# Kernel optimization log

Measured on AMD Instinct MI355X. Metric: run time of the kernel, lower is better.

Reference implementation:

```python
import jax, jax.numpy as jnp
import numpy as np

B, N, DIM, IN_DIM, H = 8, 3136, 147, 64, 1
HD = IN_DIM // H          # per-head value/key dim = 64
MLP_HID = int(IN_DIM * 1.0)
EPS = 1e-5


def _ln(x, w, b):
    m = jnp.mean(x, axis=-1, keepdims=True)
    v = jnp.mean((x - m) ** 2, axis=-1, keepdims=True)
    return (x - m) / jnp.sqrt(v + EPS) * w + b


def setup_inputs() -> dict:
    key = jax.random.key(0)
    ks = jax.random.split(key, 12)
    r = lambda k, shp, s=0.02: (jax.random.normal(k, shp, dtype=jnp.float32) * s)
    return {
        "x": jax.random.normal(ks[0], (B, N, DIM), dtype=jnp.float32),
        "norm1_w": jnp.ones((DIM,), jnp.float32),
        "norm1_b": jnp.zeros((DIM,), jnp.float32),
        "qkv_w": r(ks[1], (3 * IN_DIM, DIM)),
        "scale": jnp.full((H,), (DIM // H) ** -0.5, dtype=jnp.float32),
        "proj_w": r(ks[2], (IN_DIM, IN_DIM)),
        "proj_b": jnp.zeros((IN_DIM,), jnp.float32),
        "norm2_w": jnp.ones((IN_DIM,), jnp.float32),
        "norm2_b": jnp.zeros((IN_DIM,), jnp.float32),
        "fc1_w": r(ks[3], (MLP_HID, IN_DIM)),
        "fc1_b": jnp.zeros((MLP_HID,), jnp.float32),
        "fc2_w": r(ks[4], (IN_DIM, MLP_HID)),
        "fc2_b": jnp.zeros((IN_DIM,), jnp.float32),
    }


def reference(x, norm1_w, norm1_b, qkv_w, scale, proj_w, proj_b,
              norm2_w, norm2_b, fc1_w, fc1_b, fc2_w, fc2_b):
    h = _ln(x, norm1_w, norm1_b)                               # [B,N,DIM]
    qkv = jnp.einsum('bnc,oc->bno', h, qkv_w)                  # [B,N,3*IN_DIM]
    qkv = qkv.reshape(B, N, 3, H, HD).transpose(2, 0, 3, 1, 4)  # [3,B,H,N,HD]
    q, k, v = qkv[0], qkv[1], qkv[2]
    # LMSA: learnable per-head scale + diagonal (self) exclusion mask
    attn = jnp.einsum('bhid,bhjd->bhij', q, k) * scale[None, :, None, None]
    eye = jnp.eye(N, dtype=bool)
    attn = jnp.where(eye[None, None], -jnp.inf, attn)
    attn = jax.nn.softmax(attn, axis=-1)
    o = jnp.einsum('bhij,bhjd->bhid', attn, v)                 # [B,H,N,HD]
    o = o.transpose(0, 2, 1, 3).reshape(B, N, IN_DIM)
    o = jnp.einsum('bnd,od->bno', o, proj_w) + proj_b
    # num_heads == 1 -> residual is v itself
    x_attn = v[:, 0] + o                                       # [B,N,IN_DIM]
    h2 = _ln(x_attn, norm2_w, norm2_b)
    h2 = jax.nn.gelu(jnp.einsum('bnd,hd->bnh', h2, fc1_w) + fc1_b,
                     approximate=False)
    h2 = jnp.einsum('bnh,oh->bno', h2, fc2_w) + fc2_b
    return x_attn + h2
```

## Files before the change

### kernel.cpp

```cpp
#include <hip/hip_runtime.h>
#include <math.h>

#define B_    8
#define N_    3136
#define DIM_  147
#define KP_   160
#define TOK_  (B_*N_)
#define QKV3_ 192

typedef __attribute__((ext_vector_type(4))) float f32x4;
typedef __attribute__((ext_vector_type(4))) unsigned int u32x4;
typedef __attribute__((ext_vector_type(8))) short short8;

static __device__ __forceinline__ unsigned short f2b(float f){
  unsigned int u = __float_as_uint(f);
  u += 0x7fffu + ((u >> 16) & 1u);
  return (unsigned short)(u >> 16);
}
static __device__ __forceinline__ unsigned short f2b_t(float f){
  return (unsigned short)(__float_as_uint(f) >> 16);
}

__global__ __launch_bounds__(256) void k_prep(const float* __restrict__ qkvw,
                                              const float* __restrict__ projw,
                                              const float* __restrict__ fc1w,
                                              const float* __restrict__ fc2w,
                                              unsigned short* __restrict__ wp,
                                              unsigned short* __restrict__ wpj,
                                              unsigned short* __restrict__ w1b,
                                              unsigned short* __restrict__ w2b){
  int idx = blockIdx.x*256 + threadIdx.x;
  if(idx < QKV3_*KP_){
    int n = idx / KP_, k = idx - n*KP_;
    wp[idx] = f2b((k < DIM_) ? qkvw[n*DIM_ + k] : 0.f);
  }
  if(idx < 4096){
    wpj[idx] = f2b(projw[idx]);
    w1b[idx] = f2b(fc1w[idx]);
    w2b[idx] = f2b(fc2w[idx]);
  }
}

__global__ __launch_bounds__(256) void k_ln1(const float* __restrict__ x,
                                             const float* __restrict__ w1,
                                             const float* __restrict__ b1,
                                             unsigned short* __restrict__ hn){
  int t    = blockIdx.x*4 + (threadIdx.x >> 6);
  int lane = threadIdx.x & 63;
  const float* xr = x + (size_t)t*DIM_;
  float x0 = xr[lane];
  float x1 = xr[lane+64];
  float x2 = (lane < 19) ? xr[lane+128] : 0.f;
  float s  = x0+x1+x2;
  float sq = x0*x0 + x1*x1 + x2*x2;
  for(int d=1; d<64; d<<=1){ s += __shfl_xor(s,d,64); sq += __shfl_xor(sq,d,64); }
  float mean = s * (1.f/DIM_);
  float var  = sq * (1.f/DIM_) - mean*mean;
  float rstd = rsqrtf(var + 1e-5f);
  unsigned short* hr = hn + (size_t)t*KP_;
  hr[lane]    = f2b((x0-mean)*rstd*w1[lane]    + b1[lane]);
  hr[lane+64] = f2b((x1-mean)*rstd*w1[lane+64] + b1[lane+64]);
  if(lane < 19)       hr[lane+128] = f2b((x2-mean)*rstd*w1[lane+128] + b1[lane+128]);
  else if(lane < 32)  hr[lane+128] = 0;
}

__global__ __launch_bounds__(256) void k_qkv(const unsigned short* __restrict__ hn,
                                             const unsigned short* __restrict__ wp,
                                             const float* __restrict__ scale,
                                             unsigned short* __restrict__ qb,
                                             unsigned short* __restrict__ kb,
                                             unsigned short* __restrict__ vtb,
                                             float* __restrict__ vf){
  __shared__ alignas(16) unsigned int Asm[64*20];
  __shared__ alignas(16) unsigned int Bsm[192*20];
  __shared__ alignas(16) unsigned short VT[64*72];
  int tid = threadIdx.x;
  int w = tid>>6, lane = tid&63, quad = lane>>4, l16 = lane&15;
  int m0 = blockIdx.x*64;
  const unsigned int* hn32 = (const unsigned int*)hn;
  const unsigned int* wp32 = (const unsigned int*)wp;
  float sc2 = scale[0] * 1.44269504089f;
  f32x4 acc[12];
  for(int i=0;i<12;i++) acc[i] = (f32x4){0.f,0.f,0.f,0.f};

  for(int kk=0; kk<5; kk++){
    __syncthreads();
    for(int rep=0; rep<4; rep++){
      int idx = rep*256 + tid;
      int row = idx>>4, col = idx&15;
      Asm[row*20+col] = hn32[(m0+row)*80 + kk*16 + col];
    }
    for(int rep=0; rep<12; rep++){
      int idx = rep*256 + tid;
      int row = idx>>4, col = idx&15;
      Bsm[row*20+col] = wp32[row*80 + kk*16 + col];
    }
    __syncthreads();
    short8 Af = *(const short8*)((const unsigned short*)Asm + (w*16+l16)*40 + quad*8);
    for(int nt=0; nt<12; nt++){
      short8 Bf = *(const short8*)((const unsigned short*)Bsm + (nt*16+l16)*40 + quad*8);
      acc[nt] = __builtin_amdgcn_mfma_f32_16x16x32_bf16(Af, Bf, acc[nt], 0,0,0);
    }
  }
  for(int nt=0; nt<12; nt++){
    int o = nt*16 + l16;
    for(int r=0; r<4; r++){
      int tl = w*16 + quad*4 + r;
      int mg = m0 + tl;
      float val = acc[nt][r];
      if(o < 64){
        qb[mg*64 + o] = f2b(val*sc2);
      } else if(o < 128){
        kb[mg*64 + (o-64)] = f2b(val);
      } else {
        int hd = o - 128;
        vf[mg*64 + hd] = val;
        VT[hd*72 + tl] = f2b(val);
      }
    }
  }
  __syncthreads();
  {
    int b = m0 / N_, n0 = m0 - b*N_;
    const unsigned int* VT32 = (const unsigned int*)VT;
    unsigned int* vg = (unsigned int*)vtb + (size_t)b*64*(N_/2) + n0/2;
    for(int rep=0; rep<8; rep++){
      int idx = rep*256 + tid; int row = idx>>5, col = idx&31;
      vg[row*(N_/2) + col] = VT32[row*36 + col];
    }
  }
}

__global__ __launch_bounds__(256) void k_attn(const unsigned short* __restrict__ qb,
                                              const unsigned short* __restrict__ kb,
                                              const unsigned short* __restrict__ vtb,
                                              float* __restrict__ Opart,
                                              float* __restrict__ lpart){
  __shared__ alignas(16) unsigned int Qs[64*36];
  __shared__ alignas(16) unsigned int Ks[64*36];
  __shared__ alignas(16) unsigned int Vs[64*36];
  __shared__ alignas(16) unsigned int Ps[64*36];
  int tid = threadIdx.x;
  int w = tid>>6, lane = tid&63, quad = lane>>4, l16 = lane&15;
  int qt = blockIdx.x, sp = blockIdx.y, b = blockIdx.z;
  int kv0 = sp*25, ntile = sp ? 24 : 25;

  {
    const u32x4* qg = (const u32x4*)(qb + ((size_t)b*N_ + qt*64)*64);
    for(int rep=0; rep<2; rep++){
      int idx = rep*256 + tid; int row = idx>>3, c4 = idx&7;
      *(u32x4*)&Qs[row*36 + c4*4] = qg[row*8 + c4];
    }
  }
  __syncthreads();
  short8 Qf[2];
  for(int kk=0; kk<2; kk++)
    Qf[kk] = *(const short8*)((const unsigned short*)Qs + (w*16+l16)*72 + kk*32 + quad*8);

  f32x4 O[4];
  for(int i=0;i<4;i++) O[i] = (f32x4){0.f,0.f,0.f,0.f};
  float lrow[4] = {0.f,0.f,0.f,0.f};
  unsigned short* Ph = (unsigned short*)Ps;

  for(int t=0; t<ntile; t++){
    int kvt = kv0 + t;
    __syncthreads();
    {
      const u32x4* kg = (const u32x4*)(kb + ((size_t)b*N_ + (size_t)kvt*64)*64);
      const u32x4* vg = (const u32x4*)vtb + (size_t)b*64*392 + (size_t)kvt*8;
      for(int rep=0; rep<2; rep++){
        int idx = rep*256 + tid; int row = idx>>3, c4 = idx&7;
        *(u32x4*)&Ks[row*36 + c4*4] = kg[row*8 + c4];
        *(u32x4*)&Vs[row*36 + c4*4] = vg[(size_t)row*392 + c4];
      }
    }
    __syncthreads();

    f32x4 S[4];
    for(int jt=0; jt<4; jt++){
      short8 Kf0 = *(const short8*)((const unsigned short*)Ks + (jt*16+l16)*72 + quad*8);
      short8 Kf1 = *(const short8*)((const unsigned short*)Ks + (jt*16+l16)*72 + 32 + quad*8);
      f32x4 z = (f32x4){0.f,0.f,0.f,0.f};
      z = __builtin_amdgcn_mfma_f32_16x16x32_bf16(Qf[0], Kf0, z, 0,0,0);
      S[jt] = __builtin_amdgcn_mfma_f32_16x16x32_bf16(Qf[1], Kf1, z, 0,0,0);
    }
    if(kvt == qt){
      for(int jt=0; jt<4; jt++){
        int c = jt*16 + l16;
        for(int r=0; r<4; r++){
          float p = (c == w*16+quad*4+r) ? 0.f : __builtin_amdgcn_exp2f(S[jt][r]);
          lrow[r] += p;
          Ph[(w*16+quad*4+r)*72 + c] = f2b_t(p);
        }
      }
    } else {
      for(int jt=0; jt<4; jt++){
        int c = jt*16 + l16;
        for(int r=0; r<4; r++){
          float p = __builtin_amdgcn_exp2f(S[jt][r]);
          lrow[r] += p;
          Ph[(w*16+quad*4+r)*72 + c] = f2b_t(p);
        }
      }
    }
    __asm__ volatile("" ::: "memory");
    short8 Pf0 = *(const short8*)(Ph + (w*16+l16)*72 + quad*8);
    short8 Pf1 = *(const short8*)(Ph + (w*16+l16)*72 + 32 + quad*8);
    for(int jt=0; jt<4; jt++){
      short8 Vf0 = *(const short8*)((const unsigned short*)Vs + (jt*16+l16)*72 + quad*8);
      short8 Vf1 = *(const short8*)((const unsigned short*)Vs + (jt*16+l16)*72 + 32 + quad*8);
      O[jt] = __builtin_amdgcn_mfma_f32_16x16x32_bf16(Pf0, Vf0, O[jt], 0,0,0);
      O[jt] = __builtin_amdgcn_mfma_f32_16x16x32_bf16(Pf1, Vf1, O[jt], 0,0,0);
    }
  }
  for(int r=0; r<4; r++){
    float lr = lrow[r];
    lr += __shfl_xor(lr,1,64); lr += __shfl_xor(lr,2,64);
    lr += __shfl_xor(lr,4,64); lr += __shfl_xor(lr,8,64);
    size_t tok = (size_t)b*N_ + qt*64 + w*16 + quad*4 + r;
    if(l16 == 0) lpart[(size_t)sp*TOK_ + tok] = lr;
    float* og = Opart + ((size_t)sp*TOK_ + tok)*64;
    for(int jt=0; jt<4; jt++) og[jt*16 + l16] = O[jt][r];
  }
}

__global__ __launch_bounds__(256) void k_mlp(const float* __restrict__ O0,
                                             const float* __restrict__ O1,
                                             const float* __restrict__ l0,
                                             const float* __restrict__ l1,
                                             const float* __restrict__ vf,
                                             const unsigned short* __restrict__ wpj,
                                             const unsigned short* __restrict__ w1b,
                                             const unsigned short* __restrict__ w2b,
                                             const float* __restrict__ projb,
                                             const float* __restrict__ n2w,
                                             const float* __restrict__ n2b,
                                             const float* __restrict__ fc1b,
                                             const float* __restrict__ fc2b,
                                             float* __restrict__ out){
  __shared__ alignas(16) unsigned int Wp32[64*36];
  __shared__ alignas(16) unsigned int W132[64*36];
  __shared__ alignas(16) unsigned int W232[64*36];
  __shared__ alignas(16) unsigned int Xs32[64*36];
  unsigned short* Wp = (unsigned short*)Wp32;
  unsigned short* W1 = (unsigned short*)W132;
  unsigned short* W2 = (unsigned short*)W232;
  unsigned short* Xs = (unsigned short*)Xs32;
  int tid = threadIdx.x;
  int w = tid>>6, lane = tid&63, quad = lane>>4, l16 = lane&15;
  int t0 = blockIdx.x*64;

  for(int rep=0; rep<2; rep++){
    int idx = rep*256 + tid; int row = idx>>3, c4 = idx&7;
    *(u32x4*)&Wp32[row*36+c4*4]  = ((const u32x4*)wpj)[row*8+c4];
    *(u32x4*)&W132[row*36+c4*4] = ((const u32x4*)w1b)[row*8+c4];
    *(u32x4*)&W232[row*36+c4*4] = ((const u32x4*)w2b)[row*8+c4];
  }
  {
    const f32x4* A0 = (const f32x4*)(O0 + (size_t)t0*64);
    const f32x4* A1 = (const f32x4*)(O1 + (size_t)t0*64);
    for(int rep=0; rep<4; rep++){
      int idx = rep*256 + tid; int row = idx>>4, c4 = idx&15;
      f32x4 a = A0[row*16+c4] + A1[row*16+c4];
      float linv = 1.f/(l0[t0+row] + l1[t0+row]);
      unsigned int p0 = ((unsigned int)f2b(a[1]*linv)<<16) | f2b(a[0]*linv);
      unsigned int p1 = ((unsigned int)f2b(a[3]*linv)<<16) | f2b(a[2]*linv);
      Xs32[row*36 + c4*2]     = p0;
      Xs32[row*36 + c4*2 + 1] = p1;
    }
  }
  __syncthreads();

  f32x4 acc[4];
  for(int i=0;i<4;i++) acc[i] = (f32x4){0.f,0.f,0.f,0.f};
  short8 Af[2];
  for(int kk=0; kk<2; kk++)
    Af[kk] = *(const short8*)(Xs + (w*16+l16)*72 + kk*32 + quad*8);
  for(int jt=0; jt<4; jt++)
    for(int kk=0; kk<2; kk++){
      short8 Bf = *(const short8*)(Wp + (jt*16+l16)*72 + kk*32 + quad*8);
      acc[jt] = __builtin_amdgcn_mfma_f32_16x16x32_bf16(Af[kk], Bf, acc[jt], 0,0,0);
    }
  float xa[4][4];
  for(int jt=0; jt<4; jt++){
    int col = jt*16 + l16;
    float pb = projb[col];
    for(int r=0; r<4; r++){
      int tg = t0 + w*16 + quad*4 + r;
      xa[jt][r] = acc[jt][r] + pb + vf[tg*64 + col];
    }
  }
  for(int r=0; r<4; r++){
    float s=0.f, sq=0.f;
    for(int jt=0; jt<4; jt++){ s += xa[jt][r]; sq += xa[jt][r]*xa[jt][r]; }
    s  += __shfl_xor(s,1,64);  s  += __shfl_xor(s,2,64);
    s  += __shfl_xor(s,4,64);  s  += __shfl_xor(s,8,64);
    sq += __shfl_xor(sq,1,64); sq += __shfl_xor(sq,2,64);
    sq += __shfl_xor(sq,4,64); sq += __shfl_xor(sq,8,64);
    float mu = s*(1.f/64.f);
    float var = sq*(1.f/64.f) - mu*mu;
    float rstd = rsqrtf(var + 1e-5f);
    for(int jt=0; jt<4; jt++){
      int col = jt*16 + l16;
      Xs[(w*16+quad*4+r)*72 + col] = f2b((xa[jt][r]-mu)*rstd*n2w[col] + n2b[col]);
    }
  }
  __syncthreads();
  f32x4 acc2[4];
  for(int i=0;i<4;i++) acc2[i] = (f32x4){0.f,0.f,0.f,0.f};
  for(int kk=0; kk<2; kk++)
    Af[kk] = *(const short8*)(Xs + (w*16+l16)*72 + kk*32 + quad*8);
  for(int jt=0; jt<4; jt++)
    for(int kk=0; kk<2; kk++){
      short8 Bf = *(const short8*)(W1 + (jt*16+l16)*72 + kk*32 + quad*8);
      acc2[jt] = __builtin_amdgcn_mfma_f32_16x16x32_bf16(Af[kk], Bf, acc2[jt], 0,0,0);
    }
  for(int jt=0; jt<4; jt++){
    int col = jt*16 + l16;
    float fb = fc1b[col];
    for(int r=0; r<4; r++){
      float g = acc2[jt][r] + fb;
      Xs[(w*16+quad*4+r)*72 + col] = f2b(0.5f*g*(1.f + erff(g*0.70710678118f)));
    }
  }
  __syncthreads();
  f32x4 acc3[4];
  for(int i=0;i<4;i++) acc3[i] = (f32x4){0.f,0.f,0.f,0.f};
  for(int kk=0; kk<2; kk++)
    Af[kk] = *(const short8*)(Xs + (w*16+l16)*72 + kk*32 + quad*8);
  for(int jt=0; jt<4; jt++)
    for(int kk=0; kk<2; kk++){
      short8 Bf = *(const short8*)(W2 + (jt*16+l16)*72 + kk*32 + quad*8);
      acc3[jt] = __builtin_amdgcn_mfma_f32_16x16x32_bf16(Af[kk], Bf, acc3[jt], 0,0,0);
    }
  for(int jt=0; jt<4; jt++){
    int col = jt*16 + l16;
    float ob2 = fc2b[col];
    for(int r=0; r<4; r++){
      int tg = t0 + w*16 + quad*4 + r;
      out[tg*64 + col] = xa[jt][r] + acc3[jt][r] + ob2;
    }
  }
}

extern "C" void kernel_launch(void* const* d_in, const int* in_sizes, int n_in,
                              void* d_out, int out_size, void* d_ws, size_t ws_size,
                              hipStream_t stream){
  const float* x     = (const float*)d_in[0];
  const float* n1w   = (const float*)d_in[1];
  const float* n1b   = (const float*)d_in[2];
  const float* qkvw  = (const float*)d_in[3];
  const float* scale = (const float*)d_in[4];
  const float* projw = (const float*)d_in[5];
  const float* projb = (const float*)d_in[6];
  const float* n2w   = (const float*)d_in[7];
  const float* n2b   = (const float*)d_in[8];
  const float* fc1w  = (const float*)d_in[9];
  const float* fc1b  = (const float*)d_in[10];
  const float* fc2w  = (const float*)d_in[11];
  const float* fc2b  = (const float*)d_in[12];

  char* base = (char*)d_ws;
  unsigned short* wp  = (unsigned short*)(base + 0);
  unsigned short* wpj = (unsigned short*)(base + 61440);
  unsigned short* w1b = (unsigned short*)(base + 69632);
  unsigned short* w2b = (unsigned short*)(base + 77824);
  unsigned short* qb  = (unsigned short*)(base + 86016);
  unsigned short* kb  = (unsigned short*)(base + 3297280);
  unsigned short* vtb = (unsigned short*)(base + 6508544);
  float*          vf  = (float*)(base + 9719808);
  unsigned short* hn  = (unsigned short*)(base + 16142336);
  float*          O0  = (float*)(base + 16142336);
  float*          O1  = (float*)(base + 22564864);
  float*          l0  = (float*)(base + 28987392);
  float*          l1  = (float*)(base + 29087744);

  hipLaunchKernelGGL(k_prep, dim3(120),      dim3(256), 0, stream,
                     qkvw, projw, fc1w, fc2w, wp, wpj, w1b, w2b);
  hipLaunchKernelGGL(k_ln1,  dim3(TOK_/4),   dim3(256), 0, stream, x, n1w, n1b, hn);
  hipLaunchKernelGGL(k_qkv,  dim3(392),      dim3(256), 0, stream, hn, wp, scale, qb, kb, vtb, vf);
  hipLaunchKernelGGL(k_attn, dim3(49,2,8),   dim3(256), 0, stream, qb, kb, vtb, O0, l0);
  hipLaunchKernelGGL(k_mlp,  dim3(392),      dim3(256), 0, stream, O0, O1, l0, l1, vf,
                     wpj, w1b, w2b, projb, n2w, n2b, fc1b, fc2b, (float*)d_out);
}
```

Measured before the change: 164.5 us.

## Fuse LN1 into QKV, restructure attention split and tiles, shrink intermediates to bf16

LayerNorm1 now runs inside the QKV kernel, with weights read straight from global memory instead of being staged through shared memory. Attention moves to 128-thread blocks with 32 queries per wave and a 4-way KV split. It computes S transposed so P stays in registers rather than round-tripping through LDS, and it swizzles K loads. Partial outputs, V residuals and intermediates are stored as bf16 to cut memory traffic, and erff is replaced by a polynomial approximation. The changes risk lower accuracy from bf16 partials and the erf approximation, plus more reduction work from the 4-way split.

After: 150.5 us. 1.09x faster.

```diff
diff --git a/kernel.cpp b/kernel.cpp
--- a/kernel.cpp
+++ b/kernel.cpp
@@ -11,14 +11,21 @@
 typedef __attribute__((ext_vector_type(4))) float f32x4;
 typedef __attribute__((ext_vector_type(4))) unsigned int u32x4;
 typedef __attribute__((ext_vector_type(8))) short short8;
+typedef union { short8 s; u32x4 u; } pk8;
 
 static __device__ __forceinline__ unsigned short f2b(float f){
   unsigned int u = __float_as_uint(f);
-  u += 0x7fffu + ((u >> 16) & 1u);
-  return (unsigned short)(u >> 16);
-}
-static __device__ __forceinline__ unsigned short f2b_t(float f){
-  return (unsigned short)(__float_as_uint(f) >> 16);
+  u += 0x7fffu + ((u>>16)&1u);
+  return (unsigned short)(u>>16);
+}
+static __device__ __forceinline__ unsigned int pk2(float a, float b){
+  return ((unsigned int)f2b(b)<<16) | (unsigned int)f2b(a);
+}
+static __device__ __forceinline__ unsigned int pk2t(float a, float b){
+  return (__float_as_uint(b) & 0xffff0000u) | (__float_as_uint(a)>>16);
+}
+static __device__ __forceinline__ float b2f(unsigned short s){
+  return __uint_as_float(((unsigned int)s)<<16);
 }
 
 __global__ __launch_bounds__(256) void k_prep(const float* __restrict__ qkvw,
@@ -41,194 +48,248 @@
   }
 }
 
-__global__ __launch_bounds__(256) void k_ln1(const float* __restrict__ x,
+__global__ __launch_bounds__(256) void k_qkv(const float* __restrict__ x,
                                              const float* __restrict__ w1,
                                              const float* __restrict__ b1,
-                                             unsigned short* __restrict__ hn){
-  int t    = blockIdx.x*4 + (threadIdx.x >> 6);
-  int lane = threadIdx.x & 63;
-  const float* xr = x + (size_t)t*DIM_;
-  float x0 = xr[lane];
-  float x1 = xr[lane+64];
-  float x2 = (lane < 19) ? xr[lane+128] : 0.f;
-  float s  = x0+x1+x2;
-  float sq = x0*x0 + x1*x1 + x2*x2;
-  for(int d=1; d<64; d<<=1){ s += __shfl_xor(s,d,64); sq += __shfl_xor(sq,d,64); }
-  float mean = s * (1.f/DIM_);
-  float var  = sq * (1.f/DIM_) - mean*mean;
-  float rstd = rsqrtf(var + 1e-5f);
-  unsigned short* hr = hn + (size_t)t*KP_;
-  hr[lane]    = f2b((x0-mean)*rstd*w1[lane]    + b1[lane]);
-  hr[lane+64] = f2b((x1-mean)*rstd*w1[lane+64] + b1[lane+64]);
-  if(lane < 19)       hr[lane+128] = f2b((x2-mean)*rstd*w1[lane+128] + b1[lane+128]);
-  else if(lane < 32)  hr[lane+128] = 0;
-}
-
-__global__ __launch_bounds__(256) void k_qkv(const unsigned short* __restrict__ hn,
                                              const unsigned short* __restrict__ wp,
                                              const float* __restrict__ scale,
                                              unsigned short* __restrict__ qb,
                                              unsigned short* __restrict__ kb,
                                              unsigned short* __restrict__ vtb,
-                                             float* __restrict__ vf){
-  __shared__ alignas(16) unsigned int Asm[64*20];
-  __shared__ alignas(16) unsigned int Bsm[192*20];
-  __shared__ alignas(16) unsigned short VT[64*72];
+                                             unsigned short* __restrict__ vfb){
+  __shared__ alignas(16) float XF[32*147];
+  __shared__ alignas(16) unsigned short A_[32*168];
+  __shared__ alignas(16) unsigned short VT[64*36];
   int tid = threadIdx.x;
   int w = tid>>6, lane = tid&63, quad = lane>>4, l16 = lane&15;
-  int m0 = blockIdx.x*64;
-  const unsigned int* hn32 = (const unsigned int*)hn;
-  const unsigned int* wp32 = (const unsigned int*)wp;
+  int t0 = blockIdx.x*32;
   float sc2 = scale[0] * 1.44269504089f;
-  f32x4 acc[12];
-  for(int i=0;i<12;i++) acc[i] = (f32x4){0.f,0.f,0.f,0.f};
-
-  for(int kk=0; kk<5; kk++){
-    __syncthreads();
-    for(int rep=0; rep<4; rep++){
-      int idx = rep*256 + tid;
-      int row = idx>>4, col = idx&15;
-      Asm[row*20+col] = hn32[(m0+row)*80 + kk*16 + col];
-    }
-    for(int rep=0; rep<12; rep++){
-      int idx = rep*256 + tid;
-      int row = idx>>4, col = idx&15;
-      Bsm[row*20+col] = wp32[row*80 + kk*16 + col];
-    }
-    __syncthreads();
-    short8 Af = *(const short8*)((const unsigned short*)Asm + (w*16+l16)*40 + quad*8);
-    for(int nt=0; nt<12; nt++){
-      short8 Bf = *(const short8*)((const unsigned short*)Bsm + (nt*16+l16)*40 + quad*8);
-      acc[nt] = __builtin_amdgcn_mfma_f32_16x16x32_bf16(Af, Bf, acc[nt], 0,0,0);
-    }
-  }
-  for(int nt=0; nt<12; nt++){
-    int o = nt*16 + l16;
-    for(int r=0; r<4; r++){
-      int tl = w*16 + quad*4 + r;
-      int mg = m0 + tl;
+
+  {
+    const float* xg = x + (size_t)t0*147;
+    for(int i=0;i<19;i++){ int f = i*256 + tid; if(f < 32*147) XF[f] = xg[f]; }
+  }
+  __syncthreads();
+  {
+    int g = tid>>3, e = tid&7;
+    float s = 0.f, sq = 0.f;
+    #pragma unroll
+    for(int i=0;i<19;i++){
+      int col = e + 8*i;
+      float v = (col < 147) ? XF[g*147 + col] : 0.f;
+      s += v; sq += v*v;
+    }
+    s  += __shfl_xor(s,1,64);  s  += __shfl_xor(s,2,64);  s  += __shfl_xor(s,4,64);
+    sq += __shfl_xor(sq,1,64); sq += __shfl_xor(sq,2,64); sq += __shfl_xor(sq,4,64);
+    float mean = s*(1.f/147.f);
+    float var  = sq*(1.f/147.f) - mean*mean;
+    float rstd = rsqrtf(var + 1e-5f);
+    #pragma unroll
+    for(int i=0;i<19;i++){
+      int col = e + 8*i;
+      if(col < 147) A_[g*168 + col] = f2b((XF[g*147+col]-mean)*rstd*w1[col] + b1[col]);
+    }
+    #pragma unroll
+    for(int i=0;i<2;i++){ int col = 147 + e + 8*i; if(col < 160) A_[g*168 + col] = 0; }
+  }
+  __syncthreads();
+  int mh = (w&1)*16, cb = (w>>1)*96;
+  short8 Af[5];
+  #pragma unroll
+  for(int kk=0;kk<5;kk++)
+    Af[kk] = *(const short8*)(A_ + (mh+l16)*168 + kk*32 + quad*8);
+  f32x4 acc[6];
+  #pragma unroll
+  for(int i=0;i<6;i++) acc[i] = (f32x4){0.f,0.f,0.f,0.f};
+  #pragma unroll
+  for(int nt=0;nt<6;nt++){
+    #pragma unroll
+    for(int kk=0;kk<5;kk++){
+      short8 Bf = *(const short8*)(wp + (size_t)(cb+nt*16+l16)*160 + kk*32 + quad*8);
+      acc[nt] = __builtin_amdgcn_mfma_f32_16x16x32_bf16(Af[kk], Bf, acc[nt], 0,0,0);
+    }
+  }
+  #pragma unroll
+  for(int nt=0;nt<6;nt++){
+    int o = cb + nt*16 + l16;
+    #pragma unroll
+    for(int r=0;r<4;r++){
+      int tl = mh + quad*4 + r;
+      int mg = t0 + tl;
       float val = acc[nt][r];
       if(o < 64){
-        qb[mg*64 + o] = f2b(val*sc2);
+        qb[(size_t)mg*64 + o] = f2b(val*sc2);
       } else if(o < 128){
-        kb[mg*64 + (o-64)] = f2b(val);
+        kb[(size_t)mg*64 + (o-64)] = f2b(val);
       } else {
         int hd = o - 128;
-        vf[mg*64 + hd] = val;
-        VT[hd*72 + tl] = f2b(val);
+        unsigned short vb = f2b(val);
+        vfb[(size_t)mg*64 + hd] = vb;
+        VT[hd*36 + tl] = vb;
       }
     }
   }
   __syncthreads();
   {
-    int b = m0 / N_, n0 = m0 - b*N_;
+    int b = t0 / N_, n0 = t0 - b*N_;
     const unsigned int* VT32 = (const unsigned int*)VT;
-    unsigned int* vg = (unsigned int*)vtb + (size_t)b*64*(N_/2) + n0/2;
-    for(int rep=0; rep<8; rep++){
-      int idx = rep*256 + tid; int row = idx>>5, col = idx&31;
-      vg[row*(N_/2) + col] = VT32[row*36 + col];
-    }
-  }
-}
-
-__global__ __launch_bounds__(256) void k_attn(const unsigned short* __restrict__ qb,
-                                              const unsigned short* __restrict__ kb,
-                                              const unsigned short* __restrict__ vtb,
-                                              float* __restrict__ Opart,
-                                              float* __restrict__ lpart){
-  __shared__ alignas(16) unsigned int Qs[64*36];
-  __shared__ alignas(16) unsigned int Ks[64*36];
-  __shared__ alignas(16) unsigned int Vs[64*36];
-  __shared__ alignas(16) unsigned int Ps[64*36];
+    unsigned int* vg = (unsigned int*)vtb + ((size_t)b*64)*(N_/2) + (n0>>1);
+    for(int rep=0;rep<4;rep++){
+      int f = rep*256 + tid;
+      int row = f>>4, c = f&15;
+      vg[(size_t)row*(N_/2) + c] = VT32[row*18 + c];
+    }
+  }
+}
+
+__global__ __launch_bounds__(128,4) void k_attn(const unsigned short* __restrict__ qb,
+                                                const unsigned short* __restrict__ kb,
+                                                const unsigned short* __restrict__ vtb,
+                                                unsigned short* __restrict__ Opart,
+                                                float* __restrict__ lpart){
+  __shared__ alignas(16) unsigned int L[2*64*36];
+  unsigned int* Ks = L;
+  unsigned int* Vs = L + 64*36;
   int tid = threadIdx.x;
   int w = tid>>6, lane = tid&63, quad = lane>>4, l16 = lane&15;
   int qt = blockIdx.x, sp = blockIdx.y, b = blockIdx.z;
-  int kv0 = sp*25, ntile = sp ? 24 : 25;
-
+  int kv0 = (sp*49)>>2, kv1 = ((sp+1)*49)>>2;
+
+  short8 Qf[2][2];
   {
-    const u32x4* qg = (const u32x4*)(qb + ((size_t)b*N_ + qt*64)*64);
-    for(int rep=0; rep<2; rep++){
-      int idx = rep*256 + tid; int row = idx>>3, c4 = idx&7;
-      *(u32x4*)&Qs[row*36 + c4*4] = qg[row*8 + c4];
-    }
-  }
-  __syncthreads();
-  short8 Qf[2];
-  for(int kk=0; kk<2; kk++)
-    Qf[kk] = *(const short8*)((const unsigned short*)Qs + (w*16+l16)*72 + kk*32 + quad*8);
-
-  f32x4 O[4];
-  for(int i=0;i<4;i++) O[i] = (f32x4){0.f,0.f,0.f,0.f};
-  float lrow[4] = {0.f,0.f,0.f,0.f};
-  unsigned short* Ph = (unsigned short*)Ps;
-
-  for(int t=0; t<ntile; t++){
-    int kvt = kv0 + t;
+    const unsigned short* qg = qb + ((size_t)b*N_ + qt*64 + w*32)*64;
+    #pragma unroll
+    for(int qs=0;qs<2;qs++)
+      #pragma unroll
+      for(int kk=0;kk<2;kk++)
+        Qf[qs][kk] = *(const short8*)(qg + (qs*16+l16)*64 + kk*32 + quad*8);
+  }
+  int koff[4], voff[4]; unsigned int ldst_[4];
+  const char* kBase = (const char*)kb + (size_t)b*N_*128;
+  const char* vBase = (const char*)vtb + (size_t)b*64*(N_*2);
+  #pragma unroll
+  for(int rr=0;rr<4;rr++){
+    int f = rr*128 + tid;
+    int p = f>>3, c = f&7;
+    int sig = (p&32)|((p&12)<<1)|((p&16)>>2)|(p&3);
+    koff[rr] = sig*128 + c*16;
+    voff[rr] = p*(N_*2) + c*16;
+    ldst_[rr] = p*36 + c*4;
+  }
+  f32x4 O[2][4];
+  #pragma unroll
+  for(int qs=0;qs<2;qs++) for(int j=0;j<4;j++) O[qs][j] = (f32x4){0.f,0.f,0.f,0.f};
+  float lr[2] = {0.f, 0.f};
+  const unsigned short* Ksh = (const unsigned short*)Ks;
+  const unsigned short* Vsh = (const unsigned short*)Vs;
+  int dloc = w*32 + l16;
+
+  for(int kvt=kv0; kvt<kv1; ++kvt){
     __syncthreads();
     {
-      const u32x4* kg = (const u32x4*)(kb + ((size_t)b*N_ + (size_t)kvt*64)*64);
-      const u32x4* vg = (const u32x4*)vtb + (size_t)b*64*392 + (size_t)kvt*8;
-      for(int rep=0; rep<2; rep++){
-        int idx = rep*256 + tid; int row = idx>>3, c4 = idx&7;
-        *(u32x4*)&Ks[row*36 + c4*4] = kg[row*8 + c4];
-        *(u32x4*)&Vs[row*36 + c4*4] = vg[(size_t)row*392 + c4];
-      }
+      const char* kbB = kBase + (size_t)kvt*8192;
+      const char* vbB = vBase + (size_t)kvt*128;
+      u32x4 tk[4], tv[4];
+      #pragma unroll
+      for(int rr=0;rr<4;rr++) tk[rr] = *(const u32x4*)(kbB + koff[rr]);
+      #pragma unroll
+      for(int rr=0;rr<4;rr++) tv[rr] = *(const u32x4*)(vbB + voff[rr]);
+      #pragma unroll
+      for(int rr=0;rr<4;rr++) *(u32x4*)&Ks[ldst_[rr]] = tk[rr];
+      #pragma unroll
+      for(int rr=0;rr<4;rr++) *(u32x4*)&Vs[ldst_[rr]] = tv[rr];
     }
     __syncthreads();
 
-    f32x4 S[4];
-    for(int jt=0; jt<4; jt++){
-      short8 Kf0 = *(const short8*)((const unsigned short*)Ks + (jt*16+l16)*72 + quad*8);
-      short8 Kf1 = *(const short8*)((const unsigned short*)Ks + (jt*16+l16)*72 + 32 + quad*8);
-      f32x4 z = (f32x4){0.f,0.f,0.f,0.f};
-      z = __builtin_amdgcn_mfma_f32_16x16x32_bf16(Qf[0], Kf0, z, 0,0,0);
-      S[jt] = __builtin_amdgcn_mfma_f32_16x16x32_bf16(Qf[1], Kf1, z, 0,0,0);
-    }
+    f32x4 S[2][4];
+    f32x4 z = (f32x4){0.f,0.f,0.f,0.f};
+    #pragma unroll
+    for(int jt=0;jt<4;jt++){
+      short8 Kf0 = *(const short8*)(Ksh + (jt*16+l16)*72 + quad*8);
+      short8 Kf1 = *(const short8*)(Ksh + (jt*16+l16)*72 + 32 + quad*8);
+      S[0][jt] = __builtin_amdgcn_mfma_f32_16x16x32_bf16(Kf0, Qf[0][0], z, 0,0,0);
+      S[0][jt] = __builtin_amdgcn_mfma_f32_16x16x32_bf16(Kf1, Qf[0][1], S[0][jt], 0,0,0);
+      S[1][jt] = __builtin_amdgcn_mfma_f32_16x16x32_bf16(Kf0, Qf[1][0], z, 0,0,0);
+      S[1][jt] = __builtin_amdgcn_mfma_f32_16x16x32_bf16(Kf1, Qf[1][1], S[1][jt], 0,0,0);
+    }
+    pk8 Pb[2][2];
     if(kvt == qt){
-      for(int jt=0; jt<4; jt++){
-        int c = jt*16 + l16;
-        for(int r=0; r<4; r++){
-          float p = (c == w*16+quad*4+r) ? 0.f : __builtin_amdgcn_exp2f(S[jt][r]);
-          lrow[r] += p;
-          Ph[(w*16+quad*4+r)*72 + c] = f2b_t(p);
+      #pragma unroll
+      for(int qs=0;qs<2;qs++){
+        int dl = dloc + qs*16;
+        float p[4][4];
+        #pragma unroll
+        for(int jt=0;jt<4;jt++){
+          int kvb = (jt>>1)*32 + (jt&1)*4 + quad*8;
+          #pragma unroll
+          for(int r=0;r<4;r++){
+            float pv = (kvb + r == dl) ? 0.f : __builtin_amdgcn_exp2f(S[qs][jt][r]);
+            p[jt][r] = pv; lr[qs] += pv;
+          }
         }
+        Pb[qs][0].u = (u32x4){ pk2t(p[0][0],p[0][1]), pk2t(p[0][2],p[0][3]),
+                               pk2t(p[1][0],p[1][1]), pk2t(p[1][2],p[1][3]) };
+        Pb[qs][1].u = (u32x4){ pk2t(p[2][0],p[2][1]), pk2t(p[2][2],p[2][3]),
+                               pk2t(p[3][0],p[3][1]), pk2t(p[3][2],p[3][3]) };
       }
     } else {
-      for(int jt=0; jt<4; jt++){
-        int c = jt*16 + l16;
-        for(int r=0; r<4; r++){
-          float p = __builtin_amdgcn_exp2f(S[jt][r]);
-          lrow[r] += p;
-          Ph[(w*16+quad*4+r)*72 + c] = f2b_t(p);
-        }
+      #pragma unroll
+      for(int qs=0;qs<2;qs++){
+        float p[4][4];
+        #pragma unroll
+        for(int jt=0;jt<4;jt++)
+          #pragma unroll
+          for(int r=0;r<4;r++){
+            float pv = __builtin_amdgcn_exp2f(S[qs][jt][r]);
+            p[jt][r] = pv; lr[qs] += pv;
+          }
+        Pb[qs][0].u = (u32x4){ pk2t(p[0][0],p[0][1]), pk2t(p[0][2],p[0][3]),
+                               pk2t(p[1][0],p[1][1]), pk2t(p[1][2],p[1][3]) };
+        Pb[qs][1].u = (u32x4){ pk2t(p[2][0],p[2][1]), pk2t(p[2][2],p[2][3]),
+                               pk2t(p[3][0],p[3][1]), pk2t(p[3][2],p[3][3]) };
       }
     }
-    __asm__ volatile("" ::: "memory");
-    short8 Pf0 = *(const short8*)(Ph + (w*16+l16)*72 + quad*8);
-    short8 Pf1 = *(const short8*)(Ph + (w*16+l16)*72 + 32 + quad*8);
-    for(int jt=0; jt<4; jt++){
-      short8 Vf0 = *(const short8*)((const unsigned short*)Vs + (jt*16+l16)*72 + quad*8);
-      short8 Vf1 = *(const short8*)((const unsigned short*)Vs + (jt*16+l16)*72 + 32 + quad*8);
-      O[jt] = __builtin_amdgcn_mfma_f32_16x16x32_bf16(Pf0, Vf0, O[jt], 0,0,0);
-      O[jt] = __builtin_amdgcn_mfma_f32_16x16x32_bf16(Pf1, Vf1, O[jt], 0,0,0);
-    }
-  }
-  for(int r=0; r<4; r++){
-    float lr = lrow[r];
-    lr += __shfl_xor(lr,1,64); lr += __shfl_xor(lr,2,64);
-    lr += __shfl_xor(lr,4,64); lr += __shfl_xor(lr,8,64);
-    size_t tok = (size_t)b*N_ + qt*64 + w*16 + quad*4 + r;
-    if(l16 == 0) lpart[(size_t)sp*TOK_ + tok] = lr;
-    float* og = Opart + ((size_t)sp*TOK_ + tok)*64;
-    for(int jt=0; jt<4; jt++) og[jt*16 + l16] = O[jt][r];
-  }
-}
-
-__global__ __launch_bounds__(256) void k_mlp(const float* __restrict__ O0,
-                                             const float* __restrict__ O1,
-                                             const float* __restrict__ l0,
-                                             const float* __restrict__ l1,
-                                             const float* __restrict__ vf,
+    #pragma unroll
+    for(int jt2=0;jt2<4;jt2++){
+      short8 Vf0 = *(const short8*)(Vsh + (jt2*16+l16)*72 + quad*8);
+      short8 Vf1 = *(const short8*)(Vsh + (jt2*16+l16)*72 + 32 + quad*8);
+      O[0][jt2] = __builtin_amdgcn_mfma_f32_16x16x32_bf16(Vf0, Pb[0][0].s, O[0][jt2], 0,0,0);
+      O[0][jt2] = __builtin_amdgcn_mfma_f32_16x16x32_bf16(Vf1, Pb[0][1].s, O[0][jt2], 0,0,0);
+      O[1][jt2] = __builtin_amdgcn_mfma_f32_16x16x32_bf16(Vf0, Pb[1][0].s, O[1][jt2], 0,0,0);
+      O[1][jt2] = __builtin_amdgcn_mfma_f32_16x16x32_bf16(Vf1, Pb[1][1].s, O[1][jt2], 0,0,0);
+    }
+  }
+  lr[0] += __shfl_xor(lr[0],16,64); lr[0] += __shfl_xor(lr[0],32,64);
+  lr[1] += __shfl_xor(lr[1],16,64); lr[1] += __shfl_xor(lr[1],32,64);
+  __syncthreads();
+  #pragma unroll
+  for(int qs=0;qs<2;qs++){
+    int q = w*32 + qs*16 + l16;
+    #pragma unroll
+    for(int jt2=0;jt2<4;jt2++){
+      L[q*36 + jt2*8 + quad*2]     = pk2(O[qs][jt2][0], O[qs][jt2][1]);
+      L[q*36 + jt2*8 + quad*2 + 1] = pk2(O[qs][jt2][2], O[qs][jt2][3]);
+    }
+  }
+  if(quad == 0){
+    size_t lbase = (size_t)sp*TOK_ + (size_t)b*N_ + qt*64 + w*32;
+    lpart[lbase + l16]      = lr[0];
+    lpart[lbase + 16 + l16] = lr[1];
+  }
+  __syncthreads();
+  {
+    unsigned int* og = (unsigned int*)(Opart + ((size_t)sp*TOK_ + (size_t)b*N_ + qt*64)*64);
+    for(int rep=0;rep<4;rep++){
+      int f = rep*128 + tid;
+      int row = f>>3, c = f&7;
+      *(u32x4*)(og + row*32 + c*4) = *(const u32x4*)&L[row*36 + c*4];
+    }
+  }
+}
+
+__global__ __launch_bounds__(128) void k_mlp(const unsigned short* __restrict__ Opart,
+                                             const float* __restrict__ lpart,
+                                             const unsigned short* __restrict__ vfb,
                                              const unsigned short* __restrict__ wpj,
                                              const unsigned short* __restrict__ w1b,
                                              const unsigned short* __restrict__ w2b,
@@ -238,61 +299,66 @@
                                              const float* __restrict__ fc1b,
                                              const float* __restrict__ fc2b,
                                              float* __restrict__ out){
-  __shared__ alignas(16) unsigned int Wp32[64*36];
-  __shared__ alignas(16) unsigned int W132[64*36];
-  __shared__ alignas(16) unsigned int W232[64*36];
-  __shared__ alignas(16) unsigned int Xs32[64*36];
-  unsigned short* Wp = (unsigned short*)Wp32;
-  unsigned short* W1 = (unsigned short*)W132;
-  unsigned short* W2 = (unsigned short*)W232;
-  unsigned short* Xs = (unsigned short*)Xs32;
+  __shared__ alignas(16) unsigned short Xs[32*72];
+  unsigned int* Xs32 = (unsigned int*)Xs;
   int tid = threadIdx.x;
   int w = tid>>6, lane = tid&63, quad = lane>>4, l16 = lane&15;
-  int t0 = blockIdx.x*64;
-
-  for(int rep=0; rep<2; rep++){
-    int idx = rep*256 + tid; int row = idx>>3, c4 = idx&7;
-    *(u32x4*)&Wp32[row*36+c4*4]  = ((const u32x4*)wpj)[row*8+c4];
-    *(u32x4*)&W132[row*36+c4*4] = ((const u32x4*)w1b)[row*8+c4];
-    *(u32x4*)&W232[row*36+c4*4] = ((const u32x4*)w2b)[row*8+c4];
-  }
-  {
-    const f32x4* A0 = (const f32x4*)(O0 + (size_t)t0*64);
-    const f32x4* A1 = (const f32x4*)(O1 + (size_t)t0*64);
-    for(int rep=0; rep<4; rep++){
-      int idx = rep*256 + tid; int row = idx>>4, c4 = idx&15;
-      f32x4 a = A0[row*16+c4] + A1[row*16+c4];
-      float linv = 1.f/(l0[t0+row] + l1[t0+row]);
-      unsigned int p0 = ((unsigned int)f2b(a[1]*linv)<<16) | f2b(a[0]*linv);
-      unsigned int p1 = ((unsigned int)f2b(a[3]*linv)<<16) | f2b(a[2]*linv);
-      Xs32[row*36 + c4*2]     = p0;
-      Xs32[row*36 + c4*2 + 1] = p1;
-    }
-  }
-  __syncthreads();
-
+  int t0 = blockIdx.x*32;
+
+  #pragma unroll
+  for(int i=0;i<2;i++){
+    int f = i*128 + tid;
+    int row = f>>3, c = f&7;
+    float lo[4] = {0,0,0,0}, hi[4] = {0,0,0,0};
+    float lsum = 0.f;
+    #pragma unroll
+    for(int s=0;s<4;s++){
+      u32x4 a = *((const u32x4*)(Opart + ((size_t)s*TOK_ + t0)*64) + row*8 + c);
+      #pragma unroll
+      for(int k=0;k<4;k++){
+        lo[k] += __uint_as_float(a[k]<<16);
+        hi[k] += __uint_as_float(a[k] & 0xffff0000u);
+      }
+      lsum += lpart[(size_t)s*TOK_ + t0 + row];
+    }
+    float linv = 1.f/lsum;
+    u32x4 o;
+    #pragma unroll
+    for(int k=0;k<4;k++) o[k] = pk2(lo[k]*linv, hi[k]*linv);
+    *(u32x4*)&Xs32[row*36 + c*4] = o;
+  }
+  __syncthreads();
+
+  short8 Af[2];
+  #pragma unroll
+  for(int kk=0;kk<2;kk++)
+    Af[kk] = *(const short8*)(Xs + (w*16+l16)*72 + kk*32 + quad*8);
   f32x4 acc[4];
+  #pragma unroll
   for(int i=0;i<4;i++) acc[i] = (f32x4){0.f,0.f,0.f,0.f};
-  short8 Af[2];
-  for(int kk=0; kk<2; kk++)
-    Af[kk] = *(const short8*)(Xs + (w*16+l16)*72 + kk*32 + quad*8);
-  for(int jt=0; jt<4; jt++)
-    for(int kk=0; kk<2; kk++){
-      short8 Bf = *(const short8*)(Wp + (jt*16+l16)*72 + kk*32 + quad*8);
+  #pragma unroll
+  for(int jt=0;jt<4;jt++)
+    #pragma unroll
+    for(int kk=0;kk<2;kk++){
+      short8 Bf = *(const short8*)(wpj + (jt*16+l16)*64 + kk*32 + quad*8);
       acc[jt] = __builtin_amdgcn_mfma_f32_16x16x32_bf16(Af[kk], Bf, acc[jt], 0,0,0);
     }
   float xa[4][4];
-  for(int jt=0; jt<4; jt++){
+  #pragma unroll
+  for(int jt=0;jt<4;jt++){
     int col = jt*16 + l16;
     float pb = projb[col];
-    for(int r=0; r<4; r++){
+    #pragma unroll
+    for(int r=0;r<4;r++){
       int tg = t0 + w*16 + quad*4 + r;
-      xa[jt][r] = acc[jt][r] + pb + vf[tg*64 + col];
-    }
-  }
-  for(int r=0; r<4; r++){
-    float s=0.f, sq=0.f;
-    for(int jt=0; jt<4; jt++){ s += xa[jt][r]; sq += xa[jt][r]*xa[jt][r]; }
+      xa[jt][r] = acc[jt][r] + pb + b2f(vfb[(size_t)tg*64 + col]);
+    }
+  }
+  #pragma unroll
+  for(int r=0;r<4;r++){
+    float s = 0.f, sq = 0.f;
+    #pragma unroll
+    for(int jt=0;jt<4;jt++){ s += xa[jt][r]; sq += xa[jt][r]*xa[jt][r]; }
     s  += __shfl_xor(s,1,64);  s  += __shfl_xor(s,2,64);
     s  += __shfl_xor(s,4,64);  s  += __shfl_xor(s,8,64);
     sq += __shfl_xor(sq,1,64); sq += __shfl_xor(sq,2,64);
@@ -300,45 +366,62 @@
     float mu = s*(1.f/64.f);
     float var = sq*(1.f/64.f) - mu*mu;
     float rstd = rsqrtf(var + 1e-5f);
-    for(int jt=0; jt<4; jt++){
+    #pragma unroll
+    for(int jt=0;jt<4;jt++){
       int col = jt*16 + l16;
       Xs[(w*16+quad*4+r)*72 + col] = f2b((xa[jt][r]-mu)*rstd*n2w[col] + n2b[col]);
     }
   }
-  __syncthreads();
+  #pragma unroll
+  for(int kk=0;kk<2;kk++)
+    Af[kk] = *(const short8*)(Xs + (w*16+l16)*72 + kk*32 + quad*8);
   f32x4 acc2[4];
+  #pragma unroll
   for(int i=0;i<4;i++) acc2[i] = (f32x4){0.f,0.f,0.f,0.f};
-  for(int kk=0; kk<2; kk++)
-    Af[kk] = *(const short8*)(Xs + (w*16+l16)*72 + kk*32 + quad*8);
-  for(int jt=0; jt<4; jt++)
-    for(int kk=0; kk<2; kk++){
-      short8 Bf = *(const short8*)(W1 + (jt*16+l16)*72 + kk*32 + quad*8);
+  #pragma unroll
+  for(int jt=0;jt<4;jt++)
+    #pragma unroll
+    for(int kk=0;kk<2;kk++){
+      short8 Bf = *(const short8*)(w1b + (jt*16+l16)*64 + kk*32 + quad*8);
       acc2[jt] = __builtin_amdgcn_mfma_f32_16x16x32_bf16(Af[kk], Bf, acc2[jt], 0,0,0);
     }
-  for(int jt=0; jt<4; jt++){
+  #pragma unroll
+  for(int jt=0;jt<4;jt++){
     int col = jt*16 + l16;
     float fb = fc1b[col];
-    for(int r=0; r<4; r++){
+    #pragma unroll
+    for(int r=0;r<4;r++){
       float g = acc2[jt][r] + fb;
-      Xs[(w*16+quad*4+r)*72 + col] = f2b(0.5f*g*(1.f + erff(g*0.70710678118f)));
-    }
-  }
-  __syncthreads();
+      float z = g*0.70710678118f;
+      float az = fabsf(z);
+      float t = 1.f/(1.f + 0.3275911f*az);
+      float poly = ((((1.061405429f*t - 1.453152027f)*t + 1.421413741f)*t - 0.284496736f)*t + 0.254829592f)*t;
+      float er = 1.f - poly*__builtin_amdgcn_exp2f(-az*az*1.44269504089f);
+      er = (z < 0.f) ? -er : er;
+      Xs[(w*16+quad*4+r)*72 + col] = f2b(0.5f*g*(1.f + er));
+    }
+  }
+  #pragma unroll
+  for(int kk=0;kk<2;kk++)
+    Af[kk] = *(const short8*)(Xs + (w*16+l16)*72 + kk*32 + quad*8);
   f32x4 acc3[4];
+  #pragma unroll
   for(int i=0;i<4;i++) acc3[i] = (f32x4){0.f,0.f,0.f,0.f};
-  for(int kk=0; kk<2; kk++)
-    Af[kk] = *(const short8*)(Xs + (w*16+l16)*72 + kk*32 + quad*8);
-  for(int jt=0; jt<4; jt++)
-    for(int kk=0; kk<2; kk++){
-      short8 Bf = *(const short8*)(W2 + (jt*16+l16)*72 + kk*32 + quad*8);
+  #pragma unroll
+  for(int jt=0;jt<4;jt++)
+    #pragma unroll
+    for(int kk=0;kk<2;kk++){
+      short8 Bf = *(const short8*)(w2b + (jt*16+l16)*64 + kk*32 + quad*8);
       acc3[jt] = __builtin_amdgcn_mfma_f32_16x16x32_bf16(Af[kk], Bf, acc3[jt], 0,0,0);
     }
-  for(int jt=0; jt<4; jt++){
+  #pragma unroll
+  for(int jt=0;jt<4;jt++){
     int col = jt*16 + l16;
     float ob2 = fc2b[col];
-    for(int r=0; r<4; r++){
+    #pragma unroll
+    for(int r=0;r<4;r++){
       int tg = t0 + w*16 + quad*4 + r;
-      out[tg*64 + col] = xa[jt][r] + acc3[jt][r] + ob2;
+      out[(size_t)tg*64 + col] = xa[jt][r] + acc3[jt][r] + ob2;
     }
   }
 }
@@ -368,18 +451,15 @@
   unsigned short* qb  = (unsigned short*)(base + 86016);
   unsigned short* kb  = (unsigned short*)(base + 3297280);
   unsigned short* vtb = (unsigned short*)(base + 6508544);
-  float*          vf  = (float*)(base + 9719808);
-  unsigned short* hn  = (unsigned short*)(base + 16142336);
-  float*          O0  = (float*)(base + 16142336);
-  float*          O1  = (float*)(base + 22564864);
-  float*          l0  = (float*)(base + 28987392);
-  float*          l1  = (float*)(base + 29087744);
+  unsigned short* vfb = (unsigned short*)(base + 9719808);
+  unsigned short* Op  = (unsigned short*)(base + 12931072);
+  float*          lp  = (float*)(base + 25776128);
 
   hipLaunchKernelGGL(k_prep, dim3(120),      dim3(256), 0, stream,
                      qkvw, projw, fc1w, fc2w, wp, wpj, w1b, w2b);
-  hipLaunchKernelGGL(k_ln1,  dim3(TOK_/4),   dim3(256), 0, stream, x, n1w, n1b, hn);
-  hipLaunchKernelGGL(k_qkv,  dim3(392),      dim3(256), 0, stream, hn, wp, scale, qb, kb, vtb, vf);
-  hipLaunchKernelGGL(k_attn, dim3(49,2,8),   dim3(256), 0, stream, qb, kb, vtb, O0, l0);
-  hipLaunchKernelGGL(k_mlp,  dim3(392),      dim3(256), 0, stream, O0, O1, l0, l1, vf,
+  hipLaunchKernelGGL(k_qkv,  dim3(TOK_/32),  dim3(256), 0, stream,
+                     x, n1w, n1b, wp, scale, qb, kb, vtb, vfb);
+  hipLaunchKernelGGL(k_attn, dim3(49,4,8),   dim3(128), 0, stream, qb, kb, vtb, Op, lp);
+  hipLaunchKernelGGL(k_mlp,  dim3(TOK_/32),  dim3(128), 0, stream, Op, lp, vfb,
                      wpj, w1b, w2b, projb, n2w, n2b, fc1b, fc2b, (float*)d_out);
 }
```
